# Kernel optimization log

Measured on AMD Instinct MI355X. Metric: run time of the kernel, lower is better.

Reference implementation:

```python
import jax, jax.numpy as jnp
import numpy as np
from jax import lax

DT = 0.042
LIF_TAU_M = 20.0
THETA_LIF = 0.05
THETA_RF = 0.05
SPIKE_GAIN = 35.0
TAU_REF = 0.25
REF_DECAY = float(np.exp(-DT / TAU_REF))

B, L, N_INP, N_HID = 32, 512, 1, 1024
RHO = 0.99
INPUT_SCALING = 1.0
GAMMA_RANGE = (2.7, 4.7)
EPS_RANGE = (4.7, 6.7)


def setup_inputs() -> dict:
    key = jax.random.key(0)
    k_x, k_h, k_i, k_b, k_g, k_e = jax.random.split(key, 6)
    x = jax.random.normal(k_x, (B, L, N_INP), dtype=jnp.float32)
    # recurrent weights: 2*(2*U-1) then spectral-radius scaling to rho
    h2h = 2.0 * (2.0 * np.asarray(jax.random.uniform(k_h, (N_HID, N_HID))) - 1.0)
    sr = np.max(np.abs(np.linalg.eigvals(h2h)))
    h2h = jnp.asarray(h2h * (RHO / sr), dtype=jnp.float32)
    x2h = jax.random.uniform(k_i, (N_INP, N_HID), dtype=jnp.float32) * INPUT_SCALING
    bias = (jax.random.uniform(k_b, (N_HID,), dtype=jnp.float32) * 2.0 - 1.0) * 0.2 + 0.05
    gamma = jax.random.uniform(k_g, (N_HID,), dtype=jnp.float32) * (GAMMA_RANGE[1] - GAMMA_RANGE[0]) + GAMMA_RANGE[0]
    epsilon = jax.random.uniform(k_e, (N_HID,), dtype=jnp.float32) * (EPS_RANGE[1] - EPS_RANGE[0]) + EPS_RANGE[0]
    return {"x": x, "x2h": x2h, "h2h": h2h, "bias": bias, "gamma": gamma, "epsilon": epsilon}


def reference(x, x2h, h2h, bias, gamma, epsilon):
    dtype = x.dtype
    b, seq_len, _ = x.shape
    n_hid = h2h.shape[0]
    z0 = jnp.zeros((b, n_hid), dtype=dtype)
    # carry: (hy, hz, s, ref_period, lif_v)
    def step(carry, xt):
        hy, hz, s, ref_period, lif_v = carry
        # input current: external drive + recurrent spike drive + bias
        cur = xt @ x2h + s @ h2h + bias  # (B, n_hid)
        lif_v = lif_v + DT * (-lif_v / LIF_TAU_M + cur)
        lif_s = (lif_v > THETA_LIF).astype(dtype)
        lif_v = lif_v - lif_s * THETA_LIF  # soft (subtractive) reset
        # HRF oscillator driven by LIF spikes (alpha = beta = 0 -> no post-spike reset)
        hz = hz + DT * (SPIKE_GAIN * lif_s - gamma * hy - epsilon * hz)
        hy = hy + DT * hz
        s_new = (hy - THETA_RF - ref_period > 0).astype(dtype)
        ref_period = ref_period * REF_DECAY + s_new
        return (hy, hz, s_new, ref_period, lif_v), s_new

    carry0 = (z0, z0, z0, z0, z0)
    _, spikes = lax.scan(step, carry0, jnp.swapaxes(x, 0, 1))  # spikes: (L, B, n_hid)
    return spikes.mean(axis=0)  # mean firing rates (B, n_hid)
```

## Files before the change

kernel.cpp:

```cpp
#include <hip/hip_runtime.h>
#include <math.h>

#define NHID    1024
#define NSTEP   512
#define NB      32
#define NSPLIT  8
#define COLS    128
#define THREADS 512
#define NWAVES  8
#define MWORDS  32

typedef float f2 __attribute__((ext_vector_type(2)));
typedef int  v4i __attribute__((vector_size(16)));

__global__ __launch_bounds__(THREADS, 1)
void coesn_kernel(const float* __restrict__ x,
                  const float* __restrict__ x2h,
                  const float* __restrict__ h2h,
                  const float* __restrict__ bias,
                  const float* __restrict__ gamma_,
                  const float* __restrict__ eps_,
                  float* __restrict__ out,
                  unsigned long long* __restrict__ masks,
                  float ref_decay)
{
#pragma clang fp contract(off)
    const int tid  = threadIdx.x;
    const int blk  = blockIdx.x;
    const int b    = blk & 31;
    const int j    = blk >> 5;
    const int w    = tid >> 6;
    const int lane = tid & 63;

    __shared__ float xs[NSTEP];
    __shared__ unsigned short idxs[NWAVES][160];
    __shared__ float part[2][NWAVES][COLS];

    for (int i = tid; i < NSTEP; i += THREADS) xs[i] = x[b * NSTEP + i];

    float w_in = 0.f, bi = 0.f, ga = 0.f, ep = 0.f;
    if (tid < COLS) {
        int col = j * COLS + tid;
        w_in = x2h[col]; bi = bias[col]; ga = gamma_[col]; ep = eps_[col];
    }

    union { const float* p; unsigned int u[2]; } cv; cv.p = h2h;
    v4i srd = { (int)cv.u[0], (int)(cv.u[1] & 0xffffu),
                (int)(NHID * NHID * 4), 0x00020000 };

    const unsigned cbase = (unsigned)(j * COLS * 4 + lane * 8);

    float hy = 0.f, hz = 0.f, ref = 0.f, lv = 0.f;
    int scount = 0;

    __syncthreads();

    for (int t = 0; t < NSTEP; ++t) {
        const int par = t & 1;
        int npad = 0;

        if (t > 0) {
            const int rpar = (t - 1) & 1;
            unsigned long long v = 0;
            if (lane < 4) {
                const unsigned long long* ap =
                    &masks[((size_t)rpar * NB + b) * MWORDS + (w << 2) + lane];
                int spin = 0;
                for (;;) {
                    v = __hip_atomic_load(ap, __ATOMIC_RELAXED,
                                          __HIP_MEMORY_SCOPE_AGENT);
                    if ((int)(v >> 32) == t) break;
                    __builtin_amdgcn_s_sleep(1);
                    if (((++spin) & 4095) == 4095)
                        (void)__hip_atomic_load(ap, __ATOMIC_ACQUIRE,
                                                __HIP_MEMORY_SCOPE_AGENT);
                }
            }
            unsigned int hv = (unsigned int)v;
            unsigned int m0 = (unsigned)__shfl((int)hv, 0, 64);
            unsigned int m1 = (unsigned)__shfl((int)hv, 1, 64);
            unsigned int m2 = (unsigned)__shfl((int)hv, 2, 64);
            unsigned int m3 = (unsigned)__shfl((int)hv, 3, 64);
            unsigned long long lo = (unsigned long long)m0 |
                                    ((unsigned long long)m1 << 32);
            unsigned long long hi = (unsigned long long)m2 |
                                    ((unsigned long long)m3 << 32);
            int cw = __popcll(lo) + __popcll(hi);
            npad = (cw + 15) & ~15;

            int p0 = lane << 1;
            int c0, bit0, bit1;
            if (lane < 32) {
                c0   = __popcll(lo & ((1ull << p0) - 1ull));
                bit0 = (int)((lo >> p0) & 1ull);
                bit1 = (int)((lo >> (p0 + 1)) & 1ull);
            } else {
                int q0 = p0 - 64;
                c0   = __popcll(lo) + __popcll(hi & ((1ull << q0) - 1ull));
                bit0 = (int)((hi >> q0) & 1ull);
                bit1 = (int)((hi >> (q0 + 1)) & 1ull);
            }
            int rowbase = w << 7;
            if (bit0) idxs[w][c0]        = (unsigned short)(rowbase + p0);
            if (bit1) idxs[w][c0 + bit0] = (unsigned short)(rowbase + p0 + 1);
            if (lane < npad - cw)
                idxs[w][cw + lane] = (unsigned short)1024;
        }

        f2 ax = {0.f, 0.f};
        for (int k = 0; k < npad; k += 16) {
            const uint4* qp = (const uint4*)&idxs[w][k];
            uint4 qa = qp[0], qb = qp[1];
            unsigned rr[16];
            rr[0]=qa.x&0xffffu; rr[1]=qa.x>>16; rr[2]=qa.y&0xffffu; rr[3]=qa.y>>16;
            rr[4]=qa.z&0xffffu; rr[5]=qa.z>>16; rr[6]=qa.w&0xffffu; rr[7]=qa.w>>16;
            rr[8]=qb.x&0xffffu; rr[9]=qb.x>>16; rr[10]=qb.y&0xffffu; rr[11]=qb.y>>16;
            rr[12]=qb.z&0xffffu; rr[13]=qb.z>>16; rr[14]=qb.w&0xffffu; rr[15]=qb.w>>16;
            f2 vv[16];
            #pragma unroll
            for (int u = 0; u < 16; ++u) {
                unsigned voff = (rr[u] << 12) + cbase;
                asm volatile("buffer_load_dwordx2 %0, %1, %2, 0 offen"
                             : "=v"(vv[u]) : "v"(voff), "s"(srd));
            }
            asm volatile("s_waitcnt vmcnt(0)" ::: "memory");
            __builtin_amdgcn_sched_barrier(0);
            #pragma unroll
            for (int u = 0; u < 16; ++u) { ax.x += vv[u].x; ax.y += vv[u].y; }
        }
        *(f2*)&part[par][w][lane << 1] = ax;
        __syncthreads();

        if (tid < COLS) {
            float rsum = 0.f;
            #pragma unroll
            for (int ww = 0; ww < NWAVES; ++ww) rsum += part[par][ww][tid];

            float xv  = xs[t];
            float pp  = xv * w_in;
            float q   = pp + rsum;
            float cur = q + bi;

            float aa = (-lv) / 20.0f;
            float bb = aa + cur;
            lv = lv + 0.042f * bb;
            float ls = (lv > 0.05f) ? 1.0f : 0.0f;
            lv = lv - ls * 0.05f;

            float t1 = 35.0f * ls;
            float t2 = ga * hy;
            float t3 = ep * hz;
            float t4 = (t1 - t2) - t3;
            hz = hz + 0.042f * t4;
            hy = hy + 0.042f * hz;

            float sv = (hy - 0.05f) - ref;
            int sp = (sv > 0.0f) ? 1 : 0;
            ref = ref * ref_decay + (sp ? 1.0f : 0.0f);
            scount += sp;

            if (t < NSTEP - 1) {
                unsigned long long bal = __ballot(sp);
                if ((tid & 31) == 0) {
                    unsigned int half = (tid & 32) ? (unsigned int)(bal >> 32)
                                                   : (unsigned int)bal;
                    unsigned long long payload =
                        (((unsigned long long)(t + 1)) << 32) | half;
                    __hip_atomic_store(
                        &masks[((size_t)par * NB + b) * MWORDS + (j << 2) + (tid >> 5)],
                        payload, __ATOMIC_RELAXED, __HIP_MEMORY_SCOPE_AGENT);
                }
            }
        }
    }

    if (tid < COLS)
        out[b * NHID + j * COLS + tid] = (float)scount * (1.0f / 512.0f);
}

extern "C" void kernel_launch(void* const* d_in, const int* in_sizes, int n_in,
                              void* d_out, int out_size, void* d_ws, size_t ws_size,
                              hipStream_t stream) {
    const float* x     = (const float*)d_in[0];
    const float* x2h   = (const float*)d_in[1];
    const float* h2h   = (const float*)d_in[2];
    const float* bias  = (const float*)d_in[3];
    const float* gamma = (const float*)d_in[4];
    const float* eps   = (const float*)d_in[5];
    float* out = (float*)d_out;

    unsigned long long* masks = (unsigned long long*)d_ws;
    hipMemsetAsync(d_ws, 0, 16384, stream);

    float ref_decay = (float)exp(-(0.042 / 0.25));

    coesn_kernel<<<NB * NSPLIT, THREADS, 0, stream>>>(
        x, x2h, h2h, bias, gamma, eps, out, masks, ref_decay);
}
```

Before: 2.336 ms.

## Use 32-bit tagged 16-bit mask words and wave prefix-scan compaction

Each spike-mask publication becomes a 32-bit word holding a 16-bit step tag and 16 spike bits, replacing the 64-bit words with a 32-bit tag. Each wave now polls 8 words per step instead of 4. Compaction of active rows now uses a wave-wide shfl_up prefix scan instead of popcount over 128-bit masks, and the index list stores precomputed byte offsets as ints. The spin loop sleeps longer between polls, which lowers polling traffic but may delay waking up on the critical inter-block handoff.

After: 2.461 ms. 1.05x slower.

```diff
diff --git a/kernel.cpp b/kernel.cpp
--- a/kernel.cpp
+++ b/kernel.cpp
@@ -5,10 +5,8 @@
 #define NSTEP   512
 #define NB      32
 #define NSPLIT  8
-#define COLS    128
 #define THREADS 512
 #define NWAVES  8
-#define MWORDS  32
 
 typedef float f2 __attribute__((ext_vector_type(2)));
 typedef int  v4i __attribute__((vector_size(16)));
@@ -21,7 +19,7 @@
                   const float* __restrict__ gamma_,
                   const float* __restrict__ eps_,
                   float* __restrict__ out,
-                  unsigned long long* __restrict__ masks,
+                  unsigned int* __restrict__ masks,
                   float ref_decay)
 {
 #pragma clang fp contract(off)
@@ -33,22 +31,23 @@
     const int lane = tid & 63;
 
     __shared__ float xs[NSTEP];
-    __shared__ unsigned short idxs[NWAVES][160];
-    __shared__ float part[2][NWAVES][COLS];
+    __shared__ int   idxs[NWAVES][144];
+    __shared__ float part[2][NWAVES][128];
 
     for (int i = tid; i < NSTEP; i += THREADS) xs[i] = x[b * NSTEP + i];
 
     float w_in = 0.f, bi = 0.f, ga = 0.f, ep = 0.f;
-    if (tid < COLS) {
-        int col = j * COLS + tid;
+    if (tid < 128) {
+        int col = j * 128 + tid;
         w_in = x2h[col]; bi = bias[col]; ga = gamma_[col]; ep = eps_[col];
     }
 
-    union { const float* p; unsigned int u[2]; } cv; cv.p = h2h;
+    union { const float* p; unsigned u[2]; } cv; cv.p = h2h;
     v4i srd = { (int)cv.u[0], (int)(cv.u[1] & 0xffffu),
                 (int)(NHID * NHID * 4), 0x00020000 };
+    const int cbase = j * 512 + lane * 8;
 
-    const unsigned cbase = (unsigned)(j * COLS * 4 + lane * 8);
+    int* offw = idxs[w];
 
     float hy = 0.f, hz = 0.f, ref = 0.f, lv = 0.f;
     int scount = 0;
@@ -60,78 +59,59 @@
         int npad = 0;
 
         if (t > 0) {
-            const int rpar = (t - 1) & 1;
-            unsigned long long v = 0;
-            if (lane < 4) {
-                const unsigned long long* ap =
-                    &masks[((size_t)rpar * NB + b) * MWORDS + (w << 2) + lane];
+            unsigned v = 0;
+            if (lane < 8) {
+                const unsigned* ap =
+                    masks + ((b * 2 + par) << 6) + (w << 3) + lane;
                 int spin = 0;
                 for (;;) {
                     v = __hip_atomic_load(ap, __ATOMIC_RELAXED,
                                           __HIP_MEMORY_SCOPE_AGENT);
-                    if ((int)(v >> 32) == t) break;
-                    __builtin_amdgcn_s_sleep(1);
-                    if (((++spin) & 4095) == 4095)
+                    if ((v >> 16) == (unsigned)t) break;
+                    __builtin_amdgcn_s_sleep(2);
+                    if (((++spin) & 1023) == 0)
                         (void)__hip_atomic_load(ap, __ATOMIC_ACQUIRE,
                                                 __HIP_MEMORY_SCOPE_AGENT);
                 }
             }
-            unsigned int hv = (unsigned int)v;
-            unsigned int m0 = (unsigned)__shfl((int)hv, 0, 64);
-            unsigned int m1 = (unsigned)__shfl((int)hv, 1, 64);
-            unsigned int m2 = (unsigned)__shfl((int)hv, 2, 64);
-            unsigned int m3 = (unsigned)__shfl((int)hv, 3, 64);
-            unsigned long long lo = (unsigned long long)m0 |
-                                    ((unsigned long long)m1 << 32);
-            unsigned long long hi = (unsigned long long)m2 |
-                                    ((unsigned long long)m3 << 32);
-            int cw = __popcll(lo) + __popcll(hi);
-            npad = (cw + 15) & ~15;
-
-            int p0 = lane << 1;
-            int c0, bit0, bit1;
-            if (lane < 32) {
-                c0   = __popcll(lo & ((1ull << p0) - 1ull));
-                bit0 = (int)((lo >> p0) & 1ull);
-                bit1 = (int)((lo >> (p0 + 1)) & 1ull);
-            } else {
-                int q0 = p0 - 64;
-                c0   = __popcll(lo) + __popcll(hi & ((1ull << q0) - 1ull));
-                bit0 = (int)((hi >> q0) & 1ull);
-                bit1 = (int)((hi >> (q0 + 1)) & 1ull);
+            unsigned word = (unsigned)__shfl((int)v, lane >> 3, 64);
+            unsigned bits = (word >> ((lane & 7) << 1)) & 3u;
+            int pc  = (int)((bits & 1u) + (bits >> 1));
+            int inc = pc;
+            #pragma unroll
+            for (int d = 1; d < 64; d <<= 1) {
+                int y = __shfl_up(inc, d, 64);
+                if (lane >= d) inc += y;
             }
-            int rowbase = w << 7;
-            if (bit0) idxs[w][c0]        = (unsigned short)(rowbase + p0);
-            if (bit1) idxs[w][c0 + bit0] = (unsigned short)(rowbase + p0 + 1);
-            if (lane < npad - cw)
-                idxs[w][cw + lane] = (unsigned short)1024;
+            int total = __shfl(inc, 63, 64);
+            int off   = inc - pc;
+            int row0  = (w << 7) + (lane << 1);
+            if (bits & 1u) offw[off] = row0 << 12;
+            if (bits & 2u) offw[off + (int)(bits & 1u)] = (row0 + 1) << 12;
+            npad = (total + 15) & ~15;
+            if (lane < npad - total)
+                offw[total + lane] = NHID << 12;
         }
 
-        f2 ax = {0.f, 0.f};
+        float ax = 0.f, ay = 0.f;
         for (int k = 0; k < npad; k += 16) {
-            const uint4* qp = (const uint4*)&idxs[w][k];
-            uint4 qa = qp[0], qb = qp[1];
-            unsigned rr[16];
-            rr[0]=qa.x&0xffffu; rr[1]=qa.x>>16; rr[2]=qa.y&0xffffu; rr[3]=qa.y>>16;
-            rr[4]=qa.z&0xffffu; rr[5]=qa.z>>16; rr[6]=qa.w&0xffffu; rr[7]=qa.w>>16;
-            rr[8]=qb.x&0xffffu; rr[9]=qb.x>>16; rr[10]=qb.y&0xffffu; rr[11]=qb.y>>16;
-            rr[12]=qb.z&0xffffu; rr[13]=qb.z>>16; rr[14]=qb.w&0xffffu; rr[15]=qb.w>>16;
+            int ro[16];
+            #pragma unroll
+            for (int i = 0; i < 16; ++i) ro[i] = offw[k + i];
             f2 vv[16];
             #pragma unroll
-            for (int u = 0; u < 16; ++u) {
-                unsigned voff = (rr[u] << 12) + cbase;
+            for (int i = 0; i < 16; ++i)
                 asm volatile("buffer_load_dwordx2 %0, %1, %2, 0 offen"
-                             : "=v"(vv[u]) : "v"(voff), "s"(srd));
-            }
+                             : "=v"(vv[i]) : "v"(ro[i] + cbase), "s"(srd));
             asm volatile("s_waitcnt vmcnt(0)" ::: "memory");
             __builtin_amdgcn_sched_barrier(0);
             #pragma unroll
-            for (int u = 0; u < 16; ++u) { ax.x += vv[u].x; ax.y += vv[u].y; }
+            for (int i = 0; i < 16; ++i) { ax += vv[i].x; ay += vv[i].y; }
         }
-        *(f2*)&part[par][w][lane << 1] = ax;
+        *(f2*)&part[par][w][lane << 1] = (f2){ax, ay};
         __syncthreads();
 
-        if (tid < COLS) {
+        if (tid < 128) {
             float rsum = 0.f;
             #pragma unroll
             for (int ww = 0; ww < NWAVES; ++ww) rsum += part[par][ww][tid];
@@ -142,8 +122,8 @@
             float cur = q + bi;
 
             float aa = (-lv) / 20.0f;
-            float bb = aa + cur;
-            lv = lv + 0.042f * bb;
+            float bb2 = aa + cur;
+            lv = lv + 0.042f * bb2;
             float ls = (lv > 0.05f) ? 1.0f : 0.0f;
             lv = lv - ls * 0.05f;
 
@@ -161,21 +141,21 @@
 
             if (t < NSTEP - 1) {
                 unsigned long long bal = __ballot(sp);
-                if ((tid & 31) == 0) {
-                    unsigned int half = (tid & 32) ? (unsigned int)(bal >> 32)
-                                                   : (unsigned int)bal;
-                    unsigned long long payload =
-                        (((unsigned long long)(t + 1)) << 32) | half;
+                if ((tid & 15) == 0) {
+                    int f = j * 8 + (tid >> 4);
+                    unsigned data =
+                        (unsigned)((bal >> (lane & 48)) & 0xFFFFull);
+                    unsigned payload = (((unsigned)(t + 1)) << 16) | data;
                     __hip_atomic_store(
-                        &masks[((size_t)par * NB + b) * MWORDS + (j << 2) + (tid >> 5)],
+                        masks + ((b * 2 + ((t + 1) & 1)) << 6) + f,
                         payload, __ATOMIC_RELAXED, __HIP_MEMORY_SCOPE_AGENT);
                 }
             }
         }
     }
 
-    if (tid < COLS)
-        out[b * NHID + j * COLS + tid] = (float)scount * (1.0f / 512.0f);
+    if (tid < 128)
+        out[b * NHID + j * 128 + tid] = (float)scount * (1.0f / 512.0f);
 }
 
 extern "C" void kernel_launch(void* const* d_in, const int* in_sizes, int n_in,
@@ -189,7 +169,7 @@
     const float* eps   = (const float*)d_in[5];
     float* out = (float*)d_out;
 
-    unsigned long long* masks = (unsigned long long*)d_ws;
+    unsigned int* masks = (unsigned int*)d_ws;
     hipMemsetAsync(d_ws, 0, 16384, stream);
 
     float ref_decay = (float)exp(-(0.042 / 0.25));
```
